# Optimization experiments

Measured on AMD Instinct MI355X. Metric: run time of the kernel, lower is better.

## Reference

```python
import jax, jax.numpy as jnp
import numpy as np


def dequant_weight(cb, idx):
    """Reconstruct weight from product-quantization codebooks.
    cb:  [C, K, sub]  codebooks
    idx: [C, out]     int codes per codebook per output row
    returns W: [out, C*sub]
    """
    C = cb.shape[0]
    gathered = cb[jnp.arange(C)[:, None], idx]          # [C, out, sub]
    W = jnp.transpose(gathered, (1, 0, 2))               # [out, C, sub]
    return W.reshape(W.shape[0], -1)                     # [out, C*sub]


def setup_inputs() -> dict:
    key = jax.random.key(0)
    ks = jax.random.split(key, 7)
    B, S, D, H, C, K = 4, 2048, 1024, 4096, 8, 256
    return {
        "x": jax.random.normal(ks[0], (B, S, D), dtype=jnp.float32),
        "cb1": jax.random.normal(ks[1], (C, K, D // C), dtype=jnp.float32) * 0.02,
        "idx1": jax.random.randint(ks[2], (C, H), 0, K, dtype=jnp.int32),
        "b1": jax.random.normal(ks[3], (H,), dtype=jnp.float32) * 0.02,
        "cb2": jax.random.normal(ks[4], (C, K, H // C), dtype=jnp.float32) * 0.02,
        "idx2": jax.random.randint(ks[5], (C, D), 0, K, dtype=jnp.int32),
        "b2": jax.random.normal(ks[6], (D,), dtype=jnp.float32) * 0.02,
    }


def reference(x, cb1, idx1, b1, cb2, idx2, b2):
    # fc1: dequantize W1 [hidden, dim] from shared codebooks, then linear
    W1 = dequant_weight(cb1, idx1)                       # [H, D]
    h = jnp.einsum("bsd,hd->bsh", x, W1) + b1            # [B, S, H]
    h = jax.nn.gelu(h, approximate=False)                # exact GELU (torch default)
    # fc2: dequantize W2 [dim, hidden], linear back to dim
    W2 = dequant_weight(cb2, idx2)                       # [D, H]
    return jnp.einsum("bsh,dh->bsd", h, W2) + b2         # [B, S, D]
```

## Files before the change

### kernel.cpp

```cpp
#include <hip/hip_runtime.h>
#include <hip/hip_bf16.h>
#include <math.h>

typedef __bf16 bf16_t;
typedef bf16_t bf16x8 __attribute__((ext_vector_type(8)));
typedef float f32x4 __attribute__((ext_vector_type(4)));

__device__ __forceinline__ void g2l16(const bf16_t* g, bf16_t* l) {
    __builtin_amdgcn_global_load_lds(
        (const __attribute__((address_space(1))) void*)g,
        (__attribute__((address_space(3))) void*)l, 16, 0, 0);
}

__global__ void prep_all(const void* __restrict__ x,
                         const void* __restrict__ cb1, const int* __restrict__ idx1,
                         const void* __restrict__ b1,
                         const void* __restrict__ cb2, const int* __restrict__ idx2,
                         const void* __restrict__ b2,
                         bf16_t* __restrict__ xb, bf16_t* __restrict__ w1b,
                         bf16_t* __restrict__ w2b, float* __restrict__ b1f,
                         float* __restrict__ b2f, int* __restrict__ flag, int M) {
    __shared__ int s_bad;
    if (threadIdx.x == 0) s_bad = 0;
    __syncthreads();
    const unsigned short* xu = (const unsigned short*)x;
    int cnt = 0;
    for (int i = threadIdx.x; i < 8192; i += 256)
        cnt += (((xu[i] >> 7) & 0xFF) >= 0x88);
    atomicAdd(&s_bad, cnt);
    __syncthreads();
    const int f32 = (s_bad > 4);
    if (blockIdx.x == 0 && threadIdx.x == 0) flag[0] = f32;

    const int T0 = (M * 1024) / 8;
    const int T1 = 4096 * 128;
    const int T2 = 1024 * 512;
    const int TB = (4096 + 1024) / 8;
    const int total = T0 + T1 + T2 + TB;
    const int t = blockIdx.x * 256 + threadIdx.x;
    const int stride = gridDim.x * 256;

    for (int i = t; i < total; i += stride) {
        if (i < T0) {
            bf16x8 o;
            if (f32) {
                const float4* p = (const float4*)x;
                float4 a = p[2 * i], b = p[2 * i + 1];
                o[0] = (bf16_t)a.x; o[1] = (bf16_t)a.y; o[2] = (bf16_t)a.z; o[3] = (bf16_t)a.w;
                o[4] = (bf16_t)b.x; o[5] = (bf16_t)b.y; o[6] = (bf16_t)b.z; o[7] = (bf16_t)b.w;
            } else {
                o = ((const bf16x8*)x)[i];
            }
            *(bf16x8*)(xb + (size_t)i * 8) = o;
        } else if (i < T0 + T1 + T2) {
            int g2 = (i >= T0 + T1);
            int ii = g2 ? (i - T0 - T1) : (i - T0);
            int rows = g2 ? 1024 : 4096;
            int logsub = g2 ? 9 : 7;
            int sub = 1 << logsub;
            const int* idx = g2 ? idx2 : idx1;
            const void* cb = g2 ? cb2 : cb1;
            bf16_t* W = g2 ? w2b : w1b;
            int r = ii >> logsub;
            int col = (ii & (sub - 1)) << 3;
            int c = col >> logsub;
            int j = col & (sub - 1);
            int code = idx[c * rows + r];
            size_t src = ((size_t)(c * 256 + code) << logsub) + j;
            bf16x8 o;
            if (f32) {
                const float* s = (const float*)cb + src;
                float4 a = *(const float4*)s;
                float4 b = *(const float4*)(s + 4);
                o[0] = (bf16_t)a.x; o[1] = (bf16_t)a.y; o[2] = (bf16_t)a.z; o[3] = (bf16_t)a.w;
                o[4] = (bf16_t)b.x; o[5] = (bf16_t)b.y; o[6] = (bf16_t)b.z; o[7] = (bf16_t)b.w;
            } else {
                o = *(const bf16x8*)((const bf16_t*)cb + src);
            }
            *(bf16x8*)(W + (size_t)r * ((size_t)sub << 3) + col) = o;
        } else {
            int g = i - (T0 + T1 + T2);
#pragma unroll
            for (int j = 0; j < 8; ++j) {
                int e = g * 8 + j;
                float v;
                const void* src = (e < 4096) ? b1 : b2;
                int k = (e < 4096) ? e : e - 4096;
                v = f32 ? ((const float*)src)[k] : (float)(((const bf16_t*)src)[k]);
                if (e < 4096) b1f[k] = v; else b2f[k] = v;
            }
        }
    }
}

template <bool GELU, bool DYNOUT>
__global__ __launch_bounds__(256, 4)
void gemm_bt(const bf16_t* __restrict__ A, const bf16_t* __restrict__ Bw,
             const float* __restrict__ bias,
             bf16_t* __restrict__ obf, float* __restrict__ of32,
             int M, int N, int K, const int* __restrict__ flag) {
    __shared__ __attribute__((aligned(16))) bf16_t sA[128 * 64];
    __shared__ __attribute__((aligned(16))) bf16_t sB[128 * 64];

    const int tid = threadIdx.x;
    const int bm = blockIdx.y << 7;
    const int bn = blockIdx.x << 7;

    const int row0 = tid >> 3;
    const int kc0 = ((tid & 7) - row0) & 7;
    const bf16_t* gA = A + (size_t)(bm + row0) * K + kc0 * 8;
    const bf16_t* gB = Bw + (size_t)(bn + row0) * K + kc0 * 8;
    bf16_t* lA = sA + tid * 8;
    bf16_t* lB = sB + tid * 8;
    const size_t pskip = (size_t)32 * K;

    const int lane = tid & 63;
    const int wave = tid >> 6;
    const int quad = lane >> 4;
    const int lr = lane & 15;
    const int wm = (wave & 1) << 6;
    const int wn = (wave >> 1) << 6;

    const int arow = wm + lr;
    const int brow = wn + lr;
    const bf16x8* pA0 = (const bf16x8*)(sA + arow * 64 + ((quad + arow) & 7) * 8);
    const bf16x8* pA1 = (const bf16x8*)(sA + arow * 64 + ((quad + 4 + arow) & 7) * 8);
    const bf16x8* pB0 = (const bf16x8*)(sB + brow * 64 + ((quad + brow) & 7) * 8);
    const bf16x8* pB1 = (const bf16x8*)(sB + brow * 64 + ((quad + 4 + brow) & 7) * 8);

    f32x4 acc[4][4] = {};

    for (int k0 = 0; k0 < K; k0 += 64) {
#pragma unroll
        for (int p = 0; p < 4; ++p) g2l16(gA + p * pskip + k0, lA + p * 2048);
#pragma unroll
        for (int p = 0; p < 4; ++p) g2l16(gB + p * pskip + k0, lB + p * 2048);
        __syncthreads();

        bf16x8 af[4], bf[4];
#pragma unroll
        for (int i = 0; i < 4; ++i) { af[i] = pA0[i * 128]; bf[i] = pB0[i * 128]; }
#pragma unroll
        for (int mi = 0; mi < 4; ++mi)
#pragma unroll
            for (int ni = 0; ni < 4; ++ni)
                acc[mi][ni] = __builtin_amdgcn_mfma_f32_16x16x32_bf16(
                    af[mi], bf[ni], acc[mi][ni], 0, 0, 0);
#pragma unroll
        for (int i = 0; i < 4; ++i) { af[i] = pA1[i * 128]; bf[i] = pB1[i * 128]; }
#pragma unroll
        for (int mi = 0; mi < 4; ++mi)
#pragma unroll
            for (int ni = 0; ni < 4; ++ni)
                acc[mi][ni] = __builtin_amdgcn_mfma_f32_16x16x32_bf16(
                    af[mi], bf[ni], acc[mi][ni], 0, 0, 0);
        __syncthreads();
    }

    const int outf32 = DYNOUT ? *flag : 0;
#pragma unroll
    for (int mi = 0; mi < 4; ++mi) {
#pragma unroll
        for (int ni = 0; ni < 4; ++ni) {
            const int n = bn + wn + ni * 16 + lr;
            const float bs = bias[n];
            f32x4 v = acc[mi][ni];
#pragma unroll
            for (int r = 0; r < 4; ++r) {
                const int m = bm + wm + mi * 16 + quad * 4 + r;
                float val = v[r] + bs;
                if (GELU) val = 0.5f * val * (1.0f + erff(val * 0.70710678118654752f));
                const size_t o = (size_t)m * N + n;
                if (DYNOUT) {
                    if (outf32) of32[o] = val;
                    else        obf[o] = (bf16_t)val;
                } else {
                    obf[o] = (bf16_t)val;
                }
            }
        }
    }
}

extern "C" void kernel_launch(void* const* d_in, const int* in_sizes, int n_in,
                              void* d_out, int out_size, void* d_ws, size_t ws_size,
                              hipStream_t stream) {
    const void* x   = d_in[0];
    const void* cb1 = d_in[1];
    const int*  idx1 = (const int*)d_in[2];
    const void* b1  = d_in[3];
    const void* cb2 = d_in[4];
    const int*  idx2 = (const int*)d_in[5];
    const void* b2  = d_in[6];

    const int D = 1024, H = 4096;
    const int M = in_sizes[0] / D;

    char* ws = (char*)d_ws;
    bf16_t* xb  = (bf16_t*)ws;
    bf16_t* w1b = (bf16_t*)(ws + (size_t)M * D * 2);
    bf16_t* hb  = (bf16_t*)((char*)w1b + (size_t)H * D * 2);
    bf16_t* w2b = (bf16_t*)((char*)hb + (size_t)M * H * 2);
    float*  b1f = (float*)((char*)w2b + (size_t)D * H * 2);
    float*  b2f = b1f + H;
    int*    flag = (int*)(b2f + D);

    prep_all<<<2048, 256, 0, stream>>>(x, cb1, idx1, b1, cb2, idx2, b2,
                                       xb, w1b, w2b, b1f, b2f, flag, M);

    dim3 g1(H / 128, M / 128);
    gemm_bt<true, false><<<g1, 256, 0, stream>>>(xb, w1b, b1f, hb, nullptr, M, H, D, flag);

    dim3 g2(D / 128, M / 128);
    gemm_bt<false, true><<<g2, 256, 0, stream>>>(hb, w2b, b2f, (bf16_t*)d_out, (float*)d_out, M, D, H, flag);
}
```

Before: 274.0 us.

## Load B operand directly into registers with prefetch, swizzle block order

```diff
diff --git a/kernel.cpp b/kernel.cpp
--- a/kernel.cpp
+++ b/kernel.cpp
@@ -94,24 +94,25 @@
 }
 
 template <bool GELU, bool DYNOUT>
-__global__ __launch_bounds__(256, 4)
+__global__ __launch_bounds__(256, 2)
 void gemm_bt(const bf16_t* __restrict__ A, const bf16_t* __restrict__ Bw,
              const float* __restrict__ bias,
              bf16_t* __restrict__ obf, float* __restrict__ of32,
              int M, int N, int K, const int* __restrict__ flag) {
     __shared__ __attribute__((aligned(16))) bf16_t sA[128 * 64];
-    __shared__ __attribute__((aligned(16))) bf16_t sB[128 * 64];
 
     const int tid = threadIdx.x;
-    const int bm = blockIdx.y << 7;
-    const int bn = blockIdx.x << 7;
+
+    const int l = blockIdx.y * gridDim.x + blockIdx.x;
+    const int grp = l / (8 * gridDim.y);
+    const int rem = l % (8 * gridDim.y);
+    const int bn = (grp * 8 + (rem & 7)) << 7;
+    const int bm = (rem >> 3) << 7;
 
     const int row0 = tid >> 3;
     const int kc0 = ((tid & 7) - row0) & 7;
     const bf16_t* gA = A + (size_t)(bm + row0) * K + kc0 * 8;
-    const bf16_t* gB = Bw + (size_t)(bn + row0) * K + kc0 * 8;
     bf16_t* lA = sA + tid * 8;
-    bf16_t* lB = sB + tid * 8;
     const size_t pskip = (size_t)32 * K;
 
     const int lane = tid & 63;
@@ -122,39 +123,56 @@
     const int wn = (wave >> 1) << 6;
 
     const int arow = wm + lr;
-    const int brow = wn + lr;
     const bf16x8* pA0 = (const bf16x8*)(sA + arow * 64 + ((quad + arow) & 7) * 8);
     const bf16x8* pA1 = (const bf16x8*)(sA + arow * 64 + ((quad + 4 + arow) & 7) * 8);
-    const bf16x8* pB0 = (const bf16x8*)(sB + brow * 64 + ((quad + brow) & 7) * 8);
-    const bf16x8* pB1 = (const bf16x8*)(sB + brow * 64 + ((quad + 4 + brow) & 7) * 8);
+
+    const bf16_t* gB = Bw + (size_t)(bn + wn + lr) * K + quad * 8;
+    const size_t bstep = (size_t)16 * K;
 
     f32x4 acc[4][4] = {};
 
+    bf16x8 b0[4], b1[4];
+#pragma unroll
+    for (int ni = 0; ni < 4; ++ni) {
+        b0[ni] = *(const bf16x8*)(gB + ni * bstep);
+        b1[ni] = *(const bf16x8*)(gB + ni * bstep + 32);
+    }
+
     for (int k0 = 0; k0 < K; k0 += 64) {
 #pragma unroll
         for (int p = 0; p < 4; ++p) g2l16(gA + p * pskip + k0, lA + p * 2048);
-#pragma unroll
-        for (int p = 0; p < 4; ++p) g2l16(gB + p * pskip + k0, lB + p * 2048);
         __syncthreads();
 
-        bf16x8 af[4], bf[4];
-#pragma unroll
-        for (int i = 0; i < 4; ++i) { af[i] = pA0[i * 128]; bf[i] = pB0[i * 128]; }
+        bf16x8 nb0[4], nb1[4];
+        if (k0 + 64 < K) {
+#pragma unroll
+            for (int ni = 0; ni < 4; ++ni) {
+                nb0[ni] = *(const bf16x8*)(gB + ni * bstep + k0 + 64);
+                nb1[ni] = *(const bf16x8*)(gB + ni * bstep + k0 + 96);
+            }
+        }
+
+        bf16x8 af[4];
+#pragma unroll
+        for (int i = 0; i < 4; ++i) af[i] = pA0[i * 128];
 #pragma unroll
         for (int mi = 0; mi < 4; ++mi)
 #pragma unroll
             for (int ni = 0; ni < 4; ++ni)
                 acc[mi][ni] = __builtin_amdgcn_mfma_f32_16x16x32_bf16(
-                    af[mi], bf[ni], acc[mi][ni], 0, 0, 0);
-#pragma unroll
-        for (int i = 0; i < 4; ++i) { af[i] = pA1[i * 128]; bf[i] = pB1[i * 128]; }
+                    af[mi], b0[ni], acc[mi][ni], 0, 0, 0);
+#pragma unroll
+        for (int i = 0; i < 4; ++i) af[i] = pA1[i * 128];
 #pragma unroll
         for (int mi = 0; mi < 4; ++mi)
 #pragma unroll
             for (int ni = 0; ni < 4; ++ni)
                 acc[mi][ni] = __builtin_amdgcn_mfma_f32_16x16x32_bf16(
-                    af[mi], bf[ni], acc[mi][ni], 0, 0, 0);
+                    af[mi], b1[ni], acc[mi][ni], 0, 0, 0);
         __syncthreads();
+
+#pragma unroll
+        for (int ni = 0; ni < 4; ++ni) { b0[ni] = nb0[ni]; b1[ni] = nb1[ni]; }
     }
 
     const int outf32 = DYNOUT ? *flag : 0;
```

Measured after the change: 412.5 us. 1.51x slower.

## Double GEMM K-tile to 128, remap blocks per XCD, wave-reduce prep counter

Applied to the files above, without the earlier changes.

```diff
diff --git a/kernel.cpp b/kernel.cpp
--- a/kernel.cpp
+++ b/kernel.cpp
@@ -27,7 +27,9 @@
     int cnt = 0;
     for (int i = threadIdx.x; i < 8192; i += 256)
         cnt += (((xu[i] >> 7) & 0xFF) >= 0x88);
-    atomicAdd(&s_bad, cnt);
+#pragma unroll
+    for (int o = 32; o > 0; o >>= 1) cnt += __shfl_down(cnt, o, 64);
+    if ((threadIdx.x & 63) == 0) atomicAdd(&s_bad, cnt);
     __syncthreads();
     const int f32 = (s_bad > 4);
     if (blockIdx.x == 0 && threadIdx.x == 0) flag[0] = f32;
@@ -94,25 +96,30 @@
 }
 
 template <bool GELU, bool DYNOUT>
-__global__ __launch_bounds__(256, 4)
+__global__ __launch_bounds__(256, 2)
 void gemm_bt(const bf16_t* __restrict__ A, const bf16_t* __restrict__ Bw,
              const float* __restrict__ bias,
              bf16_t* __restrict__ obf, float* __restrict__ of32,
              int M, int N, int K, const int* __restrict__ flag) {
-    __shared__ __attribute__((aligned(16))) bf16_t sA[128 * 64];
-    __shared__ __attribute__((aligned(16))) bf16_t sB[128 * 64];
+    __shared__ __attribute__((aligned(16))) bf16_t sA[128 * 128];
+    __shared__ __attribute__((aligned(16))) bf16_t sB[128 * 128];
 
     const int tid = threadIdx.x;
-    const int bm = blockIdx.y << 7;
-    const int bn = blockIdx.x << 7;
-
-    const int row0 = tid >> 3;
-    const int kc0 = ((tid & 7) - row0) & 7;
+
+    const int l = blockIdx.y * gridDim.x + blockIdx.x;
+    const int xcd = l & 7;
+    const int i = l >> 3;
+    const int per = gridDim.y >> 3;
+    const int bm = (xcd * per + (i % per)) << 7;
+    const int bn = (i / per) << 7;
+
+    const int row0 = tid >> 4;
+    const int kc0 = ((tid & 15) - row0) & 15;
     const bf16_t* gA = A + (size_t)(bm + row0) * K + kc0 * 8;
     const bf16_t* gB = Bw + (size_t)(bn + row0) * K + kc0 * 8;
     bf16_t* lA = sA + tid * 8;
     bf16_t* lB = sB + tid * 8;
-    const size_t pskip = (size_t)32 * K;
+    const size_t pskip = (size_t)16 * K;
 
     const int lane = tid & 63;
     const int wave = tid >> 6;
@@ -120,40 +127,35 @@
     const int lr = lane & 15;
     const int wm = (wave & 1) << 6;
     const int wn = (wave >> 1) << 6;
-
     const int arow = wm + lr;
     const int brow = wn + lr;
-    const bf16x8* pA0 = (const bf16x8*)(sA + arow * 64 + ((quad + arow) & 7) * 8);
-    const bf16x8* pA1 = (const bf16x8*)(sA + arow * 64 + ((quad + 4 + arow) & 7) * 8);
-    const bf16x8* pB0 = (const bf16x8*)(sB + brow * 64 + ((quad + brow) & 7) * 8);
-    const bf16x8* pB1 = (const bf16x8*)(sB + brow * 64 + ((quad + 4 + brow) & 7) * 8);
 
     f32x4 acc[4][4] = {};
 
-    for (int k0 = 0; k0 < K; k0 += 64) {
-#pragma unroll
-        for (int p = 0; p < 4; ++p) g2l16(gA + p * pskip + k0, lA + p * 2048);
-#pragma unroll
-        for (int p = 0; p < 4; ++p) g2l16(gB + p * pskip + k0, lB + p * 2048);
+    for (int k0 = 0; k0 < K; k0 += 128) {
+#pragma unroll
+        for (int p = 0; p < 8; ++p) g2l16(gA + p * pskip + k0, lA + p * 2048);
+#pragma unroll
+        for (int p = 0; p < 8; ++p) g2l16(gB + p * pskip + k0, lB + p * 2048);
         __syncthreads();
 
-        bf16x8 af[4], bf[4];
-#pragma unroll
-        for (int i = 0; i < 4; ++i) { af[i] = pA0[i * 128]; bf[i] = pB0[i * 128]; }
-#pragma unroll
-        for (int mi = 0; mi < 4; ++mi)
-#pragma unroll
-            for (int ni = 0; ni < 4; ++ni)
-                acc[mi][ni] = __builtin_amdgcn_mfma_f32_16x16x32_bf16(
-                    af[mi], bf[ni], acc[mi][ni], 0, 0, 0);
-#pragma unroll
-        for (int i = 0; i < 4; ++i) { af[i] = pA1[i * 128]; bf[i] = pB1[i * 128]; }
-#pragma unroll
-        for (int mi = 0; mi < 4; ++mi)
-#pragma unroll
-            for (int ni = 0; ni < 4; ++ni)
-                acc[mi][ni] = __builtin_amdgcn_mfma_f32_16x16x32_bf16(
-                    af[mi], bf[ni], acc[mi][ni], 0, 0, 0);
+#pragma unroll
+        for (int s = 0; s < 4; ++s) {
+            bf16x8 af[4], bf[4];
+#pragma unroll
+            for (int f = 0; f < 4; ++f) {
+                const int ar = arow + f * 16;
+                const int br = brow + f * 16;
+                af[f] = *(const bf16x8*)(sA + ar * 128 + (((s * 4 + quad + ar) & 15) << 3));
+                bf[f] = *(const bf16x8*)(sB + br * 128 + (((s * 4 + quad + br) & 15) << 3));
+            }
+#pragma unroll
+            for (int mi = 0; mi < 4; ++mi)
+#pragma unroll
+                for (int ni = 0; ni < 4; ++ni)
+                    acc[mi][ni] = __builtin_amdgcn_mfma_f32_16x16x32_bf16(
+                        af[mi], bf[ni], acc[mi][ni], 0, 0, 0);
+        }
         __syncthreads();
     }
 
```

New measurement: 267.8 us. 1.02x faster.

## Widen fc1 GEMM tile to 128x256 and remap blocks per XCD for L2 reuse

Applied to the files above, without the earlier changes.

```diff
diff --git a/kernel.cpp b/kernel.cpp
--- a/kernel.cpp
+++ b/kernel.cpp
@@ -27,7 +27,9 @@
     int cnt = 0;
     for (int i = threadIdx.x; i < 8192; i += 256)
         cnt += (((xu[i] >> 7) & 0xFF) >= 0x88);
-    atomicAdd(&s_bad, cnt);
+#pragma unroll
+    for (int o = 32; o > 0; o >>= 1) cnt += __shfl_down(cnt, o, 64);
+    if ((threadIdx.x & 63) == 0) atomicAdd(&s_bad, cnt);
     __syncthreads();
     const int f32 = (s_bad > 4);
     if (blockIdx.x == 0 && threadIdx.x == 0) flag[0] = f32;
@@ -93,18 +95,24 @@
     }
 }
 
-template <bool GELU, bool DYNOUT>
-__global__ __launch_bounds__(256, 4)
+template <int NF, bool GELU, bool DYNOUT>
+__global__ __launch_bounds__(256, 2)
 void gemm_bt(const bf16_t* __restrict__ A, const bf16_t* __restrict__ Bw,
              const float* __restrict__ bias,
              bf16_t* __restrict__ obf, float* __restrict__ of32,
              int M, int N, int K, const int* __restrict__ flag) {
+    constexpr int BN = NF * 32;
     __shared__ __attribute__((aligned(16))) bf16_t sA[128 * 64];
-    __shared__ __attribute__((aligned(16))) bf16_t sB[128 * 64];
+    __shared__ __attribute__((aligned(16))) bf16_t sB[BN * 64];
 
     const int tid = threadIdx.x;
-    const int bm = blockIdx.y << 7;
-    const int bn = blockIdx.x << 7;
+
+    const int l = blockIdx.y * gridDim.x + blockIdx.x;
+    const int xcd = l & 7;
+    const int i = l >> 3;
+    const int per = gridDim.y >> 3;
+    const int bm = (xcd * per + (i % per)) << 7;
+    const int bn = (i / per) * BN;
 
     const int row0 = tid >> 3;
     const int kc0 = ((tid & 7) - row0) & 7;
@@ -119,7 +127,7 @@
     const int quad = lane >> 4;
     const int lr = lane & 15;
     const int wm = (wave & 1) << 6;
-    const int wn = (wave >> 1) << 6;
+    const int wn = (wave >> 1) * (NF * 16);
 
     const int arow = wm + lr;
     const int brow = wn + lr;
@@ -128,30 +136,34 @@
     const bf16x8* pB0 = (const bf16x8*)(sB + brow * 64 + ((quad + brow) & 7) * 8);
     const bf16x8* pB1 = (const bf16x8*)(sB + brow * 64 + ((quad + 4 + brow) & 7) * 8);
 
-    f32x4 acc[4][4] = {};
+    f32x4 acc[4][NF] = {};
 
     for (int k0 = 0; k0 < K; k0 += 64) {
 #pragma unroll
         for (int p = 0; p < 4; ++p) g2l16(gA + p * pskip + k0, lA + p * 2048);
 #pragma unroll
-        for (int p = 0; p < 4; ++p) g2l16(gB + p * pskip + k0, lB + p * 2048);
+        for (int p = 0; p < BN / 32; ++p) g2l16(gB + p * pskip + k0, lB + p * 2048);
         __syncthreads();
 
-        bf16x8 af[4], bf[4];
-#pragma unroll
-        for (int i = 0; i < 4; ++i) { af[i] = pA0[i * 128]; bf[i] = pB0[i * 128]; }
+        bf16x8 af[4], bf[NF];
+#pragma unroll
+        for (int f = 0; f < 4; ++f) af[f] = pA0[f * 128];
+#pragma unroll
+        for (int f = 0; f < NF; ++f) bf[f] = pB0[f * 128];
 #pragma unroll
         for (int mi = 0; mi < 4; ++mi)
 #pragma unroll
-            for (int ni = 0; ni < 4; ++ni)
+            for (int ni = 0; ni < NF; ++ni)
                 acc[mi][ni] = __builtin_amdgcn_mfma_f32_16x16x32_bf16(
                     af[mi], bf[ni], acc[mi][ni], 0, 0, 0);
 #pragma unroll
-        for (int i = 0; i < 4; ++i) { af[i] = pA1[i * 128]; bf[i] = pB1[i * 128]; }
+        for (int f = 0; f < 4; ++f) af[f] = pA1[f * 128];
+#pragma unroll
+        for (int f = 0; f < NF; ++f) bf[f] = pB1[f * 128];
 #pragma unroll
         for (int mi = 0; mi < 4; ++mi)
 #pragma unroll
-            for (int ni = 0; ni < 4; ++ni)
+            for (int ni = 0; ni < NF; ++ni)
                 acc[mi][ni] = __builtin_amdgcn_mfma_f32_16x16x32_bf16(
                     af[mi], bf[ni], acc[mi][ni], 0, 0, 0);
         __syncthreads();
@@ -161,7 +173,7 @@
 #pragma unroll
     for (int mi = 0; mi < 4; ++mi) {
 #pragma unroll
-        for (int ni = 0; ni < 4; ++ni) {
+        for (int ni = 0; ni < NF; ++ni) {
             const int n = bn + wn + ni * 16 + lr;
             const float bs = bias[n];
             f32x4 v = acc[mi][ni];
@@ -208,9 +220,9 @@
     prep_all<<<2048, 256, 0, stream>>>(x, cb1, idx1, b1, cb2, idx2, b2,
                                        xb, w1b, w2b, b1f, b2f, flag, M);
 
-    dim3 g1(H / 128, M / 128);
-    gemm_bt<true, false><<<g1, 256, 0, stream>>>(xb, w1b, b1f, hb, nullptr, M, H, D, flag);
+    dim3 g1(H / 256, M / 128);
+    gemm_bt<8, true, false><<<g1, 256, 0, stream>>>(xb, w1b, b1f, hb, nullptr, M, H, D, flag);
 
     dim3 g2(D / 128, M / 128);
-    gemm_bt<false, true><<<g2, 256, 0, stream>>>(hb, w2b, b2f, (bf16_t*)d_out, (float*)d_out, M, D, H, flag);
-}
+    gemm_bt<4, false, true><<<g2, 256, 0, stream>>>(hb, w2b, b2f, (bf16_t*)d_out, (float*)d_out, M, D, H, flag);
+}
```

Measured after the change: 260.2 us. 5.0% less time.
